# Kernel tuning notes

Measured on AMD Instinct MI355X. Metric: run time of the kernel, lower is better.

Reference implementation:

```python
import jax, jax.numpy as jnp
import numpy as np

D_MODEL = 1024
N_HEADS = 16


def setup_inputs() -> dict:
    key = jax.random.key(0)
    k1, k2, k3, k4, k5 = jax.random.split(key, 5)
    B, L, D = 2, 2048, D_MODEL
    scale = 1.0 / np.sqrt(D)
    return {
        "x": jax.random.normal(k1, (B, L, D), dtype=jnp.float32),
        "W_attn": jax.random.normal(k2, (D, 3 * D), dtype=jnp.float32) * scale,
        "b_attn": jax.random.normal(k3, (3 * D,), dtype=jnp.float32) * 0.02,
        "W_proj": jax.random.normal(k4, (D, D), dtype=jnp.float32) * scale,
        "b_proj": jax.random.normal(k5, (D,), dtype=jnp.float32) * 0.02,
    }


def reference(x, W_attn, b_attn, W_proj, b_proj):
    B, L, D = x.shape
    H = N_HEADS
    Dh = D // H
    qkv = x @ W_attn + b_attn  # [B, L, 3D]
    # Original torch code (faithfully reproduced bug): after splitting q,k,v,
    # q and v are overwritten with k, so q = k = v = the key projection.
    k = qkv[:, :, D:2 * D]
    kh = k.reshape(B, L, H, Dh).transpose(0, 2, 1, 3)  # [B, H, L, Dh]
    att = jnp.einsum("bhqd,bhkd->bhqk", kh, kh) / np.sqrt(Dh)
    att = jax.nn.softmax(att, axis=3)
    out = jnp.einsum("bhqk,bhkd->bhqd", att, kh)  # [B, H, L, Dh]
    out = out.transpose(0, 2, 1, 3).reshape(B, L, D)
    return out @ W_proj + b_proj
```

## Files before the change

### kernel.cpp

```cpp
#include <hip/hip_runtime.h>

#define L_SEQ 2048
#define DM    1024
#define NH    16
#define DH    64
#define BLM   4096

typedef __bf16 bf16x8 __attribute__((ext_vector_type(8)));
typedef float  f32x4  __attribute__((ext_vector_type(4)));

#define MFMA(a,b,c) __builtin_amdgcn_mfma_f32_16x16x32_bf16(a,b,c,0,0,0)

__device__ __forceinline__ unsigned short f2b(float x) {
    unsigned int u = __builtin_bit_cast(unsigned int, x);
    u = (u + 0x7fffu + ((u >> 16) & 1u)) >> 16;
    return (unsigned short)u;
}

typedef __attribute__((address_space(1))) unsigned int GU32;
typedef __attribute__((address_space(3))) unsigned int LU32;
__device__ __forceinline__ void async16(const void* g, void* l) {
    __builtin_amdgcn_global_load_lds((GU32*)g, (LU32*)l, 16, 0, 0);
}

__global__ __launch_bounds__(256) void conv_x(const float* __restrict__ in,
                                              unsigned short* __restrict__ out, int n8) {
    int i = blockIdx.x * 256 + threadIdx.x;
    if (i >= n8) return;
    float4 a = ((const float4*)in)[i * 2];
    float4 b = ((const float4*)in)[i * 2 + 1];
    uint4 v;
    v.x = (unsigned)f2b(a.x) | ((unsigned)f2b(a.y) << 16);
    v.y = (unsigned)f2b(a.z) | ((unsigned)f2b(a.w) << 16);
    v.z = (unsigned)f2b(b.x) | ((unsigned)f2b(b.y) << 16);
    v.w = (unsigned)f2b(b.z) | ((unsigned)f2b(b.w) << 16);
    ((uint4*)out)[i] = v;
}

__global__ __launch_bounds__(256) void transpose_w(const float* __restrict__ W, int ld, int coff,
                                                   unsigned short* __restrict__ out) {
    __shared__ float t[32][33];
    int k0 = blockIdx.x * 32, n0 = blockIdx.y * 32;
    int tx = threadIdx.x & 31, ty = threadIdx.x >> 5;
    #pragma unroll
    for (int i = 0; i < 4; i++) {
        int k = k0 + ty + i * 8;
        t[ty + i * 8][tx] = W[(size_t)k * ld + coff + n0 + tx];
    }
    __syncthreads();
    #pragma unroll
    for (int i = 0; i < 4; i++) {
        int n = n0 + ty + i * 8;
        out[(size_t)n * DM + k0 + tx] = f2b(t[tx][ty + i * 8]);
    }
}

__global__ __launch_bounds__(256) void transpose_k(const unsigned short* __restrict__ kb,
                                                   unsigned short* __restrict__ kt) {
    __shared__ unsigned short t[64][66];
    int l0 = blockIdx.x * 64;
    int bh = blockIdx.y;
    int b = bh >> 4, h = bh & 15;
    int c = threadIdx.x & 63, r4 = threadIdx.x >> 6;
    #pragma unroll
    for (int i = 0; i < 16; i++) {
        int l = r4 + i * 4;
        t[l][c] = kb[(size_t)(b * L_SEQ + l0 + l) * DM + h * DH + c];
    }
    __syncthreads();
    #pragma unroll
    for (int i = 0; i < 16; i++) {
        int d = r4 + i * 4;
        kt[(size_t)(bh * DH + d) * L_SEQ + l0 + c] = t[c][d];
    }
}

template <int OUT_BF16>
__global__ __launch_bounds__(256) void gemm_bt(const unsigned short* __restrict__ A,
                                               const unsigned short* __restrict__ BT,
                                               const float* __restrict__ bias,
                                               void* __restrict__ Cv) {
    __shared__ __align__(16) unsigned short lA[128 * 32];
    __shared__ __align__(16) unsigned short lB[64 * 32];
    const int bm = blockIdx.x, bn = blockIdx.y;
    const int tid = threadIdx.x, wid = tid >> 6, lane = tid & 63;
    const int wr = wid >> 1, wc = wid & 1;
    const int lg = lane >> 4, lc = lane & 15;
    const int srow = lane >> 2, scol = (lane & 3) * 8;

    f32x4 acc[4][2];
    #pragma unroll
    for (int m = 0; m < 4; m++)
        #pragma unroll
        for (int n = 0; n < 2; n++) acc[m][n] = (f32x4){0.f, 0.f, 0.f, 0.f};

    const unsigned short* gA = A + (size_t)bm * 128 * DM;
    const unsigned short* gB = BT + (size_t)bn * 64 * DM;

    for (int kk = 0; kk < DM; kk += 32) {
        __syncthreads();
        async16(gA + (size_t)(wid * 32 + srow) * DM + kk + scol,       lA + wid * 1024);
        async16(gA + (size_t)(wid * 32 + 16 + srow) * DM + kk + scol,  lA + wid * 1024 + 512);
        async16(gB + (size_t)(wid * 16 + srow) * DM + kk + scol,       lB + wid * 512);
        __syncthreads();

        bf16x8 af[4], bfv[2];
        #pragma unroll
        for (int m = 0; m < 4; m++)
            af[m] = *(const bf16x8*)(lA + (wr * 64 + m * 16 + lc) * 32 + lg * 8);
        #pragma unroll
        for (int n = 0; n < 2; n++)
            bfv[n] = *(const bf16x8*)(lB + (wc * 32 + n * 16 + lc) * 32 + lg * 8);
        #pragma unroll
        for (int m = 0; m < 4; m++)
            #pragma unroll
            for (int n = 0; n < 2; n++)
                acc[m][n] = MFMA(af[m], bfv[n], acc[m][n]);
    }

    #pragma unroll
    for (int m = 0; m < 4; m++) {
        int grow = bm * 128 + wr * 64 + m * 16 + lg * 4;
        #pragma unroll
        for (int n = 0; n < 2; n++) {
            int gcol = bn * 64 + wc * 32 + n * 16 + lc;
            float bs = bias[gcol];
            #pragma unroll
            for (int r = 0; r < 4; r++) {
                float v = acc[m][n][r] + bs;
                if (OUT_BF16)
                    ((unsigned short*)Cv)[(size_t)(grow + r) * DM + gcol] = f2b(v);
                else
                    ((float*)Cv)[(size_t)(grow + r) * DM + gcol] = v;
            }
        }
    }
}

__global__ __launch_bounds__(512) void attn_kernel(const unsigned short* __restrict__ kb,
                                                   const unsigned short* __restrict__ kt,
                                                   unsigned short* __restrict__ ob) {
    const int qblk = blockIdx.x, h = blockIdx.y, b = blockIdx.z;
    const int tid = threadIdx.x, wid = tid >> 6, lane = tid & 63;
    const int lg = lane >> 4, lc = lane & 15;
    const int q0 = qblk * 128 + wid * 16;
    const int bh = b * NH + h;

    __shared__ __align__(16) unsigned short kT[2][64 * 64];
    __shared__ __align__(16) unsigned short vT[2][64 * 64];
    __shared__ __align__(16) unsigned short p_lds[8][16][72];

    const int srow = wid * 8 + (lane >> 3);
    const int sc = (lane & 7) ^ (srow & 7);
    const unsigned short* gK = kb + (size_t)(b * L_SEQ + srow) * DM + h * DH + sc * 8;
    const unsigned short* gV = kt + (size_t)(bh * DH + srow) * L_SEQ + sc * 8;

    bf16x8 a_q[2];
    {
        const unsigned short* base = kb + (size_t)(b * L_SEQ + q0 + lc) * DM + h * DH;
        a_q[0] = *(const bf16x8*)(base + lg * 8);
        a_q[1] = *(const bf16x8*)(base + 32 + lg * 8);
    }

    float m_run[4], l_run[4];
    f32x4 o_acc[4];
    #pragma unroll
    for (int r = 0; r < 4; r++) { m_run[r] = -3.0e38f; l_run[r] = 0.f; }
    #pragma unroll
    for (int dt = 0; dt < 4; dt++) o_acc[dt] = (f32x4){0.f, 0.f, 0.f, 0.f};

    async16(gK, &kT[0][wid * 512]);
    async16(gV, &vT[0][wid * 512]);
    __syncthreads();

    int cur = 0;
    const int NT = L_SEQ / 64;
    for (int t = 0; t < NT; ++t) {
        if (t + 1 < NT) {
            int k0n = (t + 1) * 64;
            async16(gK + (size_t)k0n * DM, &kT[cur ^ 1][wid * 512]);
            async16(gV + k0n,              &vT[cur ^ 1][wid * 512]);
        }

        f32x4 s[4];
        #pragma unroll
        for (int nt = 0; nt < 4; nt++) {
            const int r = nt * 16 + lc, x = r & 7;
            const unsigned short* kbase = &kT[cur][r * 64];
            bf16x8 b0 = *(const bf16x8*)(kbase + ((lg    ) ^ x) * 8);
            bf16x8 b1 = *(const bf16x8*)(kbase + ((lg + 4) ^ x) * 8);
            f32x4 a = (f32x4){0.f, 0.f, 0.f, 0.f};
            a = MFMA(a_q[0], b0, a);
            a = MFMA(a_q[1], b1, a);
            s[nt] = a * 0.125f;
        }

        float tmax[4];
        #pragma unroll
        for (int r = 0; r < 4; r++)
            tmax[r] = fmaxf(fmaxf(s[0][r], s[1][r]), fmaxf(s[2][r], s[3][r]));
        #pragma unroll
        for (int off = 1; off < 16; off <<= 1)
            #pragma unroll
            for (int r = 0; r < 4; r++)
                tmax[r] = fmaxf(tmax[r], __shfl_xor(tmax[r], off));

        float corr[4], psum[4];
        unsigned short pb[4][4];
        #pragma unroll
        for (int r = 0; r < 4; r++) {
            float mn = fmaxf(m_run[r], tmax[r]);
            corr[r] = __expf(m_run[r] - mn);
            m_run[r] = mn;
            psum[r] = 0.f;
        }
        #pragma unroll
        for (int nt = 0; nt < 4; nt++)
            #pragma unroll
            for (int r = 0; r < 4; r++) {
                float p = __expf(s[nt][r] - m_run[r]);
                psum[r] += p;
                pb[nt][r] = f2b(p);
            }
        #pragma unroll
        for (int off = 1; off < 16; off <<= 1)
            #pragma unroll
            for (int r = 0; r < 4; r++)
                psum[r] += __shfl_xor(psum[r], off);
        #pragma unroll
        for (int r = 0; r < 4; r++) l_run[r] = l_run[r] * corr[r] + psum[r];
        #pragma unroll
        for (int dt = 0; dt < 4; dt++)
            #pragma unroll
            for (int r = 0; r < 4; r++) o_acc[dt][r] *= corr[r];

        #pragma unroll
        for (int nt = 0; nt < 4; nt++)
            #pragma unroll
            for (int r = 0; r < 4; r++)
                p_lds[wid][lg * 4 + r][nt * 16 + lc] = pb[nt][r];
        asm volatile("s_waitcnt lgkmcnt(0)" ::: "memory");

        #pragma unroll
        for (int ks = 0; ks < 2; ks++) {
            bf16x8 ap = *(const bf16x8*)(&p_lds[wid][lc][ks * 32 + lg * 8]);
            #pragma unroll
            for (int dt = 0; dt < 4; dt++) {
                const int r = dt * 16 + lc, x = r & 7;
                bf16x8 bv = *(const bf16x8*)(&vT[cur][r * 64 + ((ks * 4 + lg) ^ x) * 8]);
                o_acc[dt] = MFMA(ap, bv, o_acc[dt]);
            }
        }

        __syncthreads();
        cur ^= 1;
    }

    #pragma unroll
    for (int r = 0; r < 4; r++) {
        float inv = 1.0f / l_run[r];
        int row = q0 + lg * 4 + r;
        unsigned short* orow = ob + (size_t)(b * L_SEQ + row) * DM + h * DH;
        #pragma unroll
        for (int dt = 0; dt < 4; dt++)
            orow[dt * 16 + lc] = f2b(o_acc[dt][r] * inv);
    }
}

extern "C" void kernel_launch(void* const* d_in, const int* in_sizes, int n_in,
                              void* d_out, int out_size, void* d_ws, size_t ws_size,
                              hipStream_t stream) {
    (void)in_sizes; (void)n_in; (void)out_size;
    const float* x      = (const float*)d_in[0];
    const float* W_attn = (const float*)d_in[1];
    const float* b_attn = (const float*)d_in[2];
    const float* W_proj = (const float*)d_in[3];
    const float* b_proj = (const float*)d_in[4];
    float* out = (float*)d_out;

    char* ws = (char*)d_ws;
    const size_t SZ_XB = (size_t)BLM * DM * 2;
    const size_t SZ_W  = (size_t)DM * DM * 2;
    unsigned short* xb  = (unsigned short*)(ws);
    unsigned short* wkT = (unsigned short*)(ws + SZ_XB);
    unsigned short* wpT = (unsigned short*)(ws + SZ_XB + SZ_W);
    unsigned short* kbf = (unsigned short*)(ws + SZ_XB + 2 * SZ_W);
    unsigned short* ktr = (unsigned short*)(ws + 2 * SZ_XB + 2 * SZ_W);
    unsigned short* obf = (unsigned short*)(ws + 3 * SZ_XB + 2 * SZ_W);
    if (ws_size < 4 * SZ_XB + 2 * SZ_W) return;

    conv_x<<<dim3(BLM * DM / 8 / 256), dim3(256), 0, stream>>>(x, xb, BLM * DM / 8);
    transpose_w<<<dim3(32, 32), dim3(256), 0, stream>>>(W_attn, 3 * DM, DM, wkT);
    transpose_w<<<dim3(32, 32), dim3(256), 0, stream>>>(W_proj, DM, 0, wpT);
    gemm_bt<1><<<dim3(BLM / 128, DM / 64), dim3(256), 0, stream>>>(xb, wkT, b_attn + DM, (void*)kbf);
    transpose_k<<<dim3(L_SEQ / 64, 32), dim3(256), 0, stream>>>(kbf, ktr);
    attn_kernel<<<dim3(L_SEQ / 128, NH, 2), dim3(512), 0, stream>>>(kbf, ktr, obf);
    gemm_bt<0><<<dim3(BLM / 128, DM / 64), dim3(256), 0, stream>>>(obf, wpT, b_proj, out);
}
```

Baseline: 227.3 us.

## Triple-buffer GEMM and attention loads, swizzle block order, lazy softmax rescale

Both the GEMM and attention kernels move from double to triple-buffered async global-to-LDS loads, with a single vmcnt wait plus barrier per iteration instead of two syncthreads. Block indices are remapped so neighbouring workgroups are interleaved, aiming for better L2 reuse. Attention folds the 1/8 scale into an FMA, skips the max-rescale unless the running max grows by a threshold (wave-uniform ballot), and computes row sums with an MFMA against a ones vector instead of shuffle reductions. Risks: the threshold-based lazy rescale can let exponentials grow large before rescaling, and the extra LDS buffers may reduce occupancy.

```diff
diff --git a/kernel.cpp b/kernel.cpp
--- a/kernel.cpp
+++ b/kernel.cpp
@@ -80,9 +80,11 @@
                                                const unsigned short* __restrict__ BT,
                                                const float* __restrict__ bias,
                                                void* __restrict__ Cv) {
-    __shared__ __align__(16) unsigned short lA[128 * 32];
-    __shared__ __align__(16) unsigned short lB[64 * 32];
-    const int bm = blockIdx.x, bn = blockIdx.y;
+    __shared__ __align__(16) unsigned short lA[3][128 * 32];
+    __shared__ __align__(16) unsigned short lB[3][64 * 32];
+    const int old = blockIdx.x + (blockIdx.y << 5);
+    const int nl = (old & 7) * 64 + (old >> 3);
+    const int bm = nl >> 4, bn = nl & 15;
     const int tid = threadIdx.x, wid = tid >> 6, lane = tid & 63;
     const int wr = wid >> 1, wc = wid & 1;
     const int lg = lane >> 4, lc = lane & 15;
@@ -97,26 +99,38 @@
     const unsigned short* gA = A + (size_t)bm * 128 * DM;
     const unsigned short* gB = BT + (size_t)bn * 64 * DM;
 
-    for (int kk = 0; kk < DM; kk += 32) {
-        __syncthreads();
-        async16(gA + (size_t)(wid * 32 + srow) * DM + kk + scol,       lA + wid * 1024);
-        async16(gA + (size_t)(wid * 32 + 16 + srow) * DM + kk + scol,  lA + wid * 1024 + 512);
-        async16(gB + (size_t)(wid * 16 + srow) * DM + kk + scol,       lB + wid * 512);
-        __syncthreads();
+#define GSTAGE(buf, kk) do { \
+    async16(gA + (size_t)(wid * 32 + srow) * DM + (kk) + scol,      lA[buf] + wid * 1024); \
+    async16(gA + (size_t)(wid * 32 + 16 + srow) * DM + (kk) + scol, lA[buf] + wid * 1024 + 512); \
+    async16(gB + (size_t)(wid * 16 + srow) * DM + (kk) + scol,      lB[buf] + wid * 512); \
+} while (0)
+
+    GSTAGE(0, 0);
+    GSTAGE(1, 32);
+    int cur = 0, pre = 2;
+    const int NT = DM / 32;
+    for (int t = 0; t < NT; ++t) {
+        if (t + 1 < NT) asm volatile("s_waitcnt vmcnt(3)\n\ts_barrier" ::: "memory");
+        else            asm volatile("s_waitcnt vmcnt(0)\n\ts_barrier" ::: "memory");
+        if (t + 2 < NT) GSTAGE(pre, (t + 2) * 32);
 
         bf16x8 af[4], bfv[2];
         #pragma unroll
         for (int m = 0; m < 4; m++)
-            af[m] = *(const bf16x8*)(lA + (wr * 64 + m * 16 + lc) * 32 + lg * 8);
+            af[m] = *(const bf16x8*)(lA[cur] + (wr * 64 + m * 16 + lc) * 32 + lg * 8);
         #pragma unroll
         for (int n = 0; n < 2; n++)
-            bfv[n] = *(const bf16x8*)(lB + (wc * 32 + n * 16 + lc) * 32 + lg * 8);
+            bfv[n] = *(const bf16x8*)(lB[cur] + (wc * 32 + n * 16 + lc) * 32 + lg * 8);
         #pragma unroll
         for (int m = 0; m < 4; m++)
             #pragma unroll
             for (int n = 0; n < 2; n++)
                 acc[m][n] = MFMA(af[m], bfv[n], acc[m][n]);
-    }
+
+        cur = (cur == 2) ? 0 : cur + 1;
+        pre = (pre == 2) ? 0 : pre + 1;
+    }
+#undef GSTAGE
 
     #pragma unroll
     for (int m = 0; m < 4; m++) {
@@ -140,15 +154,17 @@
 __global__ __launch_bounds__(512) void attn_kernel(const unsigned short* __restrict__ kb,
                                                    const unsigned short* __restrict__ kt,
                                                    unsigned short* __restrict__ ob) {
-    const int qblk = blockIdx.x, h = blockIdx.y, b = blockIdx.z;
+    const int lin = blockIdx.x + (blockIdx.y << 4) + (blockIdx.z << 8);
+    const int nl = (lin & 7) * 64 + (lin >> 3);
+    const int qblk = nl & 15, h = (nl >> 4) & 15, b = nl >> 8;
     const int tid = threadIdx.x, wid = tid >> 6, lane = tid & 63;
     const int lg = lane >> 4, lc = lane & 15;
     const int q0 = qblk * 128 + wid * 16;
     const int bh = b * NH + h;
 
-    __shared__ __align__(16) unsigned short kT[2][64 * 64];
-    __shared__ __align__(16) unsigned short vT[2][64 * 64];
-    __shared__ __align__(16) unsigned short p_lds[8][16][72];
+    __shared__ __align__(16) unsigned short kT[3][64 * 64];
+    __shared__ __align__(16) unsigned short vT[3][64 * 64];
+    __shared__ __align__(16) __bf16 p_lds[8][16][72];
 
     const int srow = wid * 8 + (lane >> 3);
     const int sc = (lane & 7) ^ (srow & 7);
@@ -162,6 +178,10 @@
         a_q[1] = *(const bf16x8*)(base + 32 + lg * 8);
     }
 
+    bf16x8 ones;
+    #pragma unroll
+    for (int i = 0; i < 8; i++) ones[i] = (__bf16)1.0f;
+
     float m_run[4], l_run[4];
     f32x4 o_acc[4];
     #pragma unroll
@@ -169,17 +189,20 @@
     #pragma unroll
     for (int dt = 0; dt < 4; dt++) o_acc[dt] = (f32x4){0.f, 0.f, 0.f, 0.f};
 
+    const int NT = L_SEQ / 64;
     async16(gK, &kT[0][wid * 512]);
     async16(gV, &vT[0][wid * 512]);
-    __syncthreads();
-
-    int cur = 0;
-    const int NT = L_SEQ / 64;
+    async16(gK + (size_t)64 * DM, &kT[1][wid * 512]);
+    async16(gV + 64,              &vT[1][wid * 512]);
+
+    int cur = 0, pre = 2;
     for (int t = 0; t < NT; ++t) {
-        if (t + 1 < NT) {
-            int k0n = (t + 1) * 64;
-            async16(gK + (size_t)k0n * DM, &kT[cur ^ 1][wid * 512]);
-            async16(gV + k0n,              &vT[cur ^ 1][wid * 512]);
+        if (t + 1 < NT) asm volatile("s_waitcnt vmcnt(2)\n\ts_barrier" ::: "memory");
+        else            asm volatile("s_waitcnt vmcnt(0)\n\ts_barrier" ::: "memory");
+        if (t + 2 < NT) {
+            int k0n = (t + 2) * 64;
+            async16(gK + (size_t)k0n * DM, &kT[pre][wid * 512]);
+            async16(gV + k0n,              &vT[pre][wid * 512]);
         }
 
         f32x4 s[4];
@@ -191,8 +214,7 @@
             bf16x8 b1 = *(const bf16x8*)(kbase + ((lg + 4) ^ x) * 8);
             f32x4 a = (f32x4){0.f, 0.f, 0.f, 0.f};
             a = MFMA(a_q[0], b0, a);
-            a = MFMA(a_q[1], b1, a);
-            s[nt] = a * 0.125f;
+            s[nt] = MFMA(a_q[1], b1, a);
         }
 
         float tmax[4];
@@ -205,45 +227,38 @@
             for (int r = 0; r < 4; r++)
                 tmax[r] = fmaxf(tmax[r], __shfl_xor(tmax[r], off));
 
-        float corr[4], psum[4];
-        unsigned short pb[4][4];
-        #pragma unroll
-        for (int r = 0; r < 4; r++) {
-            float mn = fmaxf(m_run[r], tmax[r]);
-            corr[r] = __expf(m_run[r] - mn);
-            m_run[r] = mn;
-            psum[r] = 0.f;
-        }
+        int grow = 0;
+        #pragma unroll
+        for (int r = 0; r < 4; r++) grow |= (tmax[r] > m_run[r] + 44.0f) ? 1 : 0;
+        if (__ballot(grow) != 0ull) {
+            #pragma unroll
+            for (int r = 0; r < 4; r++) {
+                float mn = fmaxf(m_run[r], tmax[r]);
+                float corr = __expf((m_run[r] - mn) * 0.125f);
+                m_run[r] = mn;
+                l_run[r] *= corr;
+                #pragma unroll
+                for (int dt = 0; dt < 4; dt++) o_acc[dt][r] *= corr;
+            }
+        }
+
+        float m8[4];
+        #pragma unroll
+        for (int r = 0; r < 4; r++) m8[r] = m_run[r] * 0.125f;
         #pragma unroll
         for (int nt = 0; nt < 4; nt++)
             #pragma unroll
             for (int r = 0; r < 4; r++) {
-                float p = __expf(s[nt][r] - m_run[r]);
-                psum[r] += p;
-                pb[nt][r] = f2b(p);
+                float p = __expf(__builtin_fmaf(s[nt][r], 0.125f, -m8[r]));
+                p_lds[wid][lg * 4 + r][nt * 16 + lc] = (__bf16)p;
             }
-        #pragma unroll
-        for (int off = 1; off < 16; off <<= 1)
-            #pragma unroll
-            for (int r = 0; r < 4; r++)
-                psum[r] += __shfl_xor(psum[r], off);
-        #pragma unroll
-        for (int r = 0; r < 4; r++) l_run[r] = l_run[r] * corr[r] + psum[r];
-        #pragma unroll
-        for (int dt = 0; dt < 4; dt++)
-            #pragma unroll
-            for (int r = 0; r < 4; r++) o_acc[dt][r] *= corr[r];
-
-        #pragma unroll
-        for (int nt = 0; nt < 4; nt++)
-            #pragma unroll
-            for (int r = 0; r < 4; r++)
-                p_lds[wid][lg * 4 + r][nt * 16 + lc] = pb[nt][r];
         asm volatile("s_waitcnt lgkmcnt(0)" ::: "memory");
 
+        f32x4 rs = (f32x4){0.f, 0.f, 0.f, 0.f};
         #pragma unroll
         for (int ks = 0; ks < 2; ks++) {
             bf16x8 ap = *(const bf16x8*)(&p_lds[wid][lc][ks * 32 + lg * 8]);
+            rs = MFMA(ap, ones, rs);
             #pragma unroll
             for (int dt = 0; dt < 4; dt++) {
                 const int r = dt * 16 + lc, x = r & 7;
@@ -251,9 +266,11 @@
                 o_acc[dt] = MFMA(ap, bv, o_acc[dt]);
             }
         }
-
-        __syncthreads();
-        cur ^= 1;
+        #pragma unroll
+        for (int r = 0; r < 4; r++) l_run[r] += rs[r];
+
+        cur = (cur == 2) ? 0 : cur + 1;
+        pre = (pre == 2) ? 0 : pre + 1;
     }
 
     #pragma unroll
```

Measured after the change: 210.2 us. 1.08x faster.
